# Kernel optimization log

Hardware: AMD Instinct MI355X
Metric: run time of the kernel (lower is better)

Reference implementation:

```python
import jax, jax.numpy as jnp
import numpy as np

D_KQ = 1024

def setup_inputs() -> dict:
    key = jax.random.key(0)
    k1, k2, k3, k4, k5 = jax.random.split(key, 5)
    x = jax.random.normal(k1, (4, 2048, 1024), dtype=jnp.float32)
    attention_mask = jax.random.randint(k2, (2048, 2048), 0, 2) == 1
    q_weights = jax.random.normal(k3, (1024, 1024), dtype=jnp.float32)
    k_weights = jax.random.normal(k4, (1024, 1024), dtype=jnp.float32)
    v_weights = jax.random.normal(k5, (1024, 1024), dtype=jnp.float32)
    return {"x": x, "attention_mask": attention_mask,
            "q_weights": q_weights, "k_weights": k_weights, "v_weights": v_weights}

def reference(x, attention_mask, q_weights, k_weights, v_weights):
    # projections: [B,S,d_in] @ [d_in,d] -> [B,S,d]
    query = x @ q_weights
    key = x @ k_weights
    value = x @ v_weights
    # scores: [B,S,S]
    attn_scores = jnp.einsum('bqd,bkd->bqk', query, key)
    masked = jnp.where(attention_mask, -jnp.inf, attn_scores)
    attn_weights = jax.nn.softmax(masked / jnp.sqrt(jnp.float32(D_KQ)), axis=-1)
    return attn_weights @ value
```

## Files before the change

kernel.cpp:

```cpp
#include <hip/hip_runtime.h>
#include <math.h>

static constexpr int BATCH = 4;
static constexpr int SEQ   = 2048;
static constexpr int DIM   = 1024;

typedef __attribute__((ext_vector_type(8))) short     bf16x8;
typedef __attribute__((ext_vector_type(4))) float     f32x4;

__device__ __forceinline__ unsigned short f2b(float v) {
    unsigned int u = __float_as_uint(v);
    u = u + 0x7fffu + ((u >> 16) & 1u);
    return (unsigned short)(u >> 16);
}
__device__ __forceinline__ float b2f(unsigned short h) {
    return __uint_as_float(((unsigned int)h) << 16);
}

__global__ __launch_bounds__(256) void convert_x_kernel(
    const float* __restrict__ X, unsigned short* __restrict__ hi,
    unsigned short* __restrict__ lo)
{
    const int i = blockIdx.x * 256 + threadIdx.x;
    const float4 v = ((const float4*)X)[i];
    ushort4 h, l;
    h.x = f2b(v.x); l.x = f2b(v.x - b2f(h.x));
    h.y = f2b(v.y); l.y = f2b(v.y - b2f(h.y));
    h.z = f2b(v.z); l.z = f2b(v.z - b2f(h.z));
    h.w = f2b(v.w); l.w = f2b(v.w - b2f(h.w));
    ((ushort4*)hi)[i] = h;
    ((ushort4*)lo)[i] = l;
}

__global__ __launch_bounds__(256) void convert_wqk_kernel(
    const float* __restrict__ Wq, const float* __restrict__ Wk,
    unsigned short* __restrict__ hi, unsigned short* __restrict__ lo)
{
    const int z = blockIdx.y;
    const float* __restrict__ W = z ? Wk : Wq;
    const int i = blockIdx.x * 256 + threadIdx.x;
    const int o = z * (DIM * DIM / 4) + i;
    const float4 v = ((const float4*)W)[i];
    ushort4 h, l;
    h.x = f2b(v.x); l.x = f2b(v.x - b2f(h.x));
    h.y = f2b(v.y); l.y = f2b(v.y - b2f(h.y));
    h.z = f2b(v.z); l.z = f2b(v.z - b2f(h.z));
    h.w = f2b(v.w); l.w = f2b(v.w - b2f(h.w));
    ((ushort4*)hi)[o] = h;
    ((ushort4*)lo)[o] = l;
}

__global__ __launch_bounds__(256) void convert_wv_kernel(
    const float* __restrict__ W, unsigned short* __restrict__ WT)
{
    __shared__ float t[32][33];
    const int n0 = blockIdx.x * 32, k0 = blockIdx.y * 32;
    const int tx = threadIdx.x & 31, ty = threadIdx.x >> 5;
#pragma unroll
    for (int i = 0; i < 4; ++i)
        t[ty + i * 8][tx] = W[(size_t)(k0 + ty + i * 8) * DIM + (n0 + tx)];
    __syncthreads();
#pragma unroll
    for (int i = 0; i < 4; ++i)
        WT[(size_t)(n0 + ty + i * 8) * DIM + (k0 + tx)] = f2b(t[tx][ty + i * 8]);
}

__global__ __launch_bounds__(256) void mask_pack_kernel(
    const int* __restrict__ mask, unsigned long long* __restrict__ Mb)
{
    const int row  = blockIdx.x;
    const int lane = threadIdx.x & 63, w = threadIdx.x >> 6;
#pragma unroll
    for (int c = w; c < SEQ / 64; c += 4) {
        const int v = mask[(size_t)row * SEQ + c * 64 + lane];
        const unsigned long long bits = __ballot(v != 0);
        if (lane == 0) Mb[(size_t)row * (SEQ / 64) + c] = bits;
    }
}

__device__ __forceinline__ void stage_async(
    const unsigned short* __restrict__ g, int gstride, int row0, int k0,
    unsigned short* lds, int tid)
{
    const int w = tid >> 6, lane = tid & 63;
    const int c = (lane & 3) ^ ((lane >> 4) & 3);
#pragma unroll
    for (int h = 0; h < 2; ++h) {
        const int row = 32 * w + 16 * h + (lane >> 2);
        const unsigned short* src = g + (size_t)(row0 + row) * gstride + k0 + 8 * c;
        unsigned short* dst = lds + (32 * w + 16 * h) * 32;
        __builtin_amdgcn_global_load_lds(
            (const __attribute__((address_space(1))) void*)src,
            (__attribute__((address_space(3))) void*)dst, 16, 0, 0);
    }
}

__device__ __forceinline__ bf16x8 fragr(const unsigned short* lds, int row, int qsw)
{
    return *(const bf16x8*)(lds + row * 32 + qsw * 8);
}

__global__ __launch_bounds__(256) void m_gemm_kernel(
    const unsigned short* __restrict__ Whi, const unsigned short* __restrict__ Wlo,
    float* __restrict__ Mtp)
{
    __shared__ unsigned short Ah[128 * 32], Al[128 * 32];
    __shared__ unsigned short Bh[128 * 32], Bl[128 * 32];

    const int tid = threadIdx.x;
    const int w = tid >> 6, lane = tid & 63;
    const int wm = (w >> 1) * 64, wn = (w & 1) * 64;
    const int m0 = blockIdx.y * 128, n0 = blockIdx.x * 128;
    const int z = blockIdx.z;

    const unsigned short* __restrict__ Ahg = Whi + (size_t)DIM * DIM;
    const unsigned short* __restrict__ Alg = Wlo + (size_t)DIM * DIM;
    const unsigned short* __restrict__ Bhg = Whi;
    const unsigned short* __restrict__ Blg = Wlo;
    float* __restrict__ Cp = Mtp + (size_t)z * DIM * DIM;

    f32x4 acc[4][4];
#pragma unroll
    for (int i = 0; i < 4; ++i)
#pragma unroll
        for (int j = 0; j < 4; ++j) acc[i][j] = (f32x4){0.f, 0.f, 0.f, 0.f};

    const int fr = lane & 15, quad = lane >> 4;
    const int qsw = quad ^ ((fr >> 2) & 3);

    for (int k0 = z * 256; k0 < z * 256 + 256; k0 += 32) {
        stage_async(Ahg, DIM, m0, k0, Ah, tid);
        stage_async(Alg, DIM, m0, k0, Al, tid);
        stage_async(Bhg, DIM, n0, k0, Bh, tid);
        stage_async(Blg, DIM, n0, k0, Bl, tid);
        __syncthreads();

        bf16x8 ah[4], al[4];
#pragma unroll
        for (int mt = 0; mt < 4; ++mt) {
            ah[mt] = fragr(Ah, wm + mt * 16 + fr, qsw);
            al[mt] = fragr(Al, wm + mt * 16 + fr, qsw);
        }
#pragma unroll
        for (int nt = 0; nt < 4; ++nt) {
            const bf16x8 bh = fragr(Bh, wn + nt * 16 + fr, qsw);
            const bf16x8 bl = fragr(Bl, wn + nt * 16 + fr, qsw);
#pragma unroll
            for (int mt = 0; mt < 4; ++mt) {
                acc[mt][nt] = __builtin_amdgcn_mfma_f32_16x16x32_bf16(ah[mt], bh, acc[mt][nt], 0, 0, 0);
                acc[mt][nt] = __builtin_amdgcn_mfma_f32_16x16x32_bf16(ah[mt], bl, acc[mt][nt], 0, 0, 0);
                acc[mt][nt] = __builtin_amdgcn_mfma_f32_16x16x32_bf16(al[mt], bh, acc[mt][nt], 0, 0, 0);
            }
        }
        __syncthreads();
    }

    const int col = lane & 15, rq = lane >> 4;
#pragma unroll
    for (int mt = 0; mt < 4; ++mt)
#pragma unroll
        for (int nt = 0; nt < 4; ++nt)
#pragma unroll
            for (int e = 0; e < 4; ++e) {
                const int m = m0 + wm + mt * 16 + rq * 4 + e;
                const int n = n0 + wn + nt * 16 + col;
                Cp[(size_t)m * DIM + n] = acc[mt][nt][e];
            }
}

__global__ __launch_bounds__(256) void m_reduce_kernel(
    const float* __restrict__ Mtp, unsigned short* __restrict__ Mthi,
    unsigned short* __restrict__ Mtlo)
{
    const int i = blockIdx.x * 256 + threadIdx.x;
    const size_t q = (size_t)DIM * DIM / 4;
    const float4 a = ((const float4*)Mtp)[i];
    const float4 b = ((const float4*)Mtp)[i + q];
    const float4 c = ((const float4*)Mtp)[i + 2 * q];
    const float4 d = ((const float4*)Mtp)[i + 3 * q];
    const float4 v = make_float4(a.x + b.x + c.x + d.x, a.y + b.y + c.y + d.y,
                                 a.z + b.z + c.z + d.z, a.w + b.w + c.w + d.w);
    ushort4 h, l;
    h.x = f2b(v.x); l.x = f2b(v.x - b2f(h.x));
    h.y = f2b(v.y); l.y = f2b(v.y - b2f(h.y));
    h.z = f2b(v.z); l.z = f2b(v.z - b2f(h.z));
    h.w = f2b(v.w); l.w = f2b(v.w - b2f(h.w));
    ((ushort4*)Mthi)[i] = h;
    ((ushort4*)Mtlo)[i] = l;
}

__global__ __launch_bounds__(256) void yv_gemm_kernel(
    const unsigned short* __restrict__ Xhi, const unsigned short* __restrict__ Xlo,
    const unsigned short* __restrict__ Mthi, const unsigned short* __restrict__ Mtlo,
    const unsigned short* __restrict__ WvT,
    unsigned short* __restrict__ Yhi, unsigned short* __restrict__ Ylo,
    unsigned short* __restrict__ Vt)
{
    __shared__ unsigned short Ah[128 * 32], Al[128 * 32];
    __shared__ unsigned short Bh[128 * 32], Bl[128 * 32];

    const int tid = threadIdx.x;
    const int w = tid >> 6, lane = tid & 63;
    const int wm = (w >> 1) * 64, wn = (w & 1) * 64;

    const int flat = blockIdx.x + (blockIdx.y << 3) + (blockIdx.z << 9);
    const int xcd = flat & 7, s = flat >> 3;
    const int cg  = xcd + ((s >> 3) << 3);
    const int n0 = (s & 7) * 128;
    const int m0 = (cg & 63) * 128;
    const int z  = cg >> 6;
    const bool full = (z == 0);

    const unsigned short* __restrict__ Bhg = full ? Mthi : WvT;
    const unsigned short* __restrict__ Blg = Mtlo;

    f32x4 acc[4][4];
#pragma unroll
    for (int i = 0; i < 4; ++i)
#pragma unroll
        for (int j = 0; j < 4; ++j) acc[i][j] = (f32x4){0.f, 0.f, 0.f, 0.f};

    const int fr = lane & 15, quad = lane >> 4;
    const int qsw = quad ^ ((fr >> 2) & 3);

    for (int k0 = 0; k0 < DIM; k0 += 32) {
        stage_async(Xhi, DIM, m0, k0, Ah, tid);
        stage_async(Bhg, DIM, n0, k0, Bh, tid);
        if (full) {
            stage_async(Xlo, DIM, m0, k0, Al, tid);
            stage_async(Blg, DIM, n0, k0, Bl, tid);
        }
        __syncthreads();

        bf16x8 ah[4], al[4];
#pragma unroll
        for (int mt = 0; mt < 4; ++mt)
            ah[mt] = fragr(Ah, wm + mt * 16 + fr, qsw);
        if (full) {
#pragma unroll
            for (int mt = 0; mt < 4; ++mt)
                al[mt] = fragr(Al, wm + mt * 16 + fr, qsw);
        }
#pragma unroll
        for (int nt = 0; nt < 4; ++nt) {
            const bf16x8 bh = fragr(Bh, wn + nt * 16 + fr, qsw);
#pragma unroll
            for (int mt = 0; mt < 4; ++mt)
                acc[mt][nt] = __builtin_amdgcn_mfma_f32_16x16x32_bf16(ah[mt], bh, acc[mt][nt], 0, 0, 0);
            if (full) {
                const bf16x8 bl = fragr(Bl, wn + nt * 16 + fr, qsw);
#pragma unroll
                for (int mt = 0; mt < 4; ++mt) {
                    acc[mt][nt] = __builtin_amdgcn_mfma_f32_16x16x32_bf16(ah[mt], bl, acc[mt][nt], 0, 0, 0);
                    acc[mt][nt] = __builtin_amdgcn_mfma_f32_16x16x32_bf16(al[mt], bh, acc[mt][nt], 0, 0, 0);
                }
            }
        }
        __syncthreads();
    }

    const int col = lane & 15, rq = lane >> 4;
    if (full) {
#pragma unroll
        for (int mt = 0; mt < 4; ++mt)
#pragma unroll
            for (int nt = 0; nt < 4; ++nt)
#pragma unroll
                for (int e = 0; e < 4; ++e) {
                    const int m = m0 + wm + mt * 16 + rq * 4 + e;
                    const int n = n0 + wn + nt * 16 + col;
                    const float v = acc[mt][nt][e];
                    const unsigned short h = f2b(v);
                    Yhi[(size_t)m * DIM + n] = h;
                    Ylo[(size_t)m * DIM + n] = f2b(v - b2f(h));
                }
    } else {
#pragma unroll
        for (int mt = 0; mt < 4; ++mt)
#pragma unroll
            for (int nt = 0; nt < 4; ++nt) {
                const int m = m0 + wm + mt * 16 + rq * 4;
                const int bb = m >> 11, sr = m & (SEQ - 1);
                const int n = n0 + wn + nt * 16 + col;
                ushort4 pk;
                pk.x = f2b(acc[mt][nt][0]);
                pk.y = f2b(acc[mt][nt][1]);
                pk.z = f2b(acc[mt][nt][2]);
                pk.w = f2b(acc[mt][nt][3]);
                *(ushort4*)(Vt + (size_t)bb * DIM * SEQ + (size_t)n * SEQ + sr) = pk;
            }
    }
}

__global__ __launch_bounds__(512, 2) void s_gemm256_kernel(
    const unsigned short* __restrict__ Yhi, const unsigned short* __restrict__ Ylo,
    const unsigned short* __restrict__ Xhi, const unsigned short* __restrict__ Xlo,
    const unsigned long long* __restrict__ Mb, float* __restrict__ Sc)
{
    extern __shared__ unsigned short smem[];

    const int tid = threadIdx.x;
    const int w = tid >> 6, lane = tid & 63;
    const int wm = (w >> 2) * 128, wn = (w & 3) * 64;

    const int flat = blockIdx.x + (blockIdx.y << 3) + (blockIdx.z << 6);
    const int lid  = ((flat & 7) << 5) | (flat >> 3);
    const int m0 = ((lid >> 3) & 7) * 256, n0 = (lid & 7) * 256;
    const int b  = lid >> 6;

    const unsigned short* __restrict__ Ahg = Yhi + (size_t)b * SEQ * DIM;
    const unsigned short* __restrict__ Alg = Ylo + (size_t)b * SEQ * DIM;
    const unsigned short* __restrict__ Bhg = Xhi + (size_t)b * SEQ * DIM;
    const unsigned short* __restrict__ Blg = Xlo + (size_t)b * SEQ * DIM;
    float* __restrict__ Sb = Sc + (size_t)b * SEQ * SEQ;

    f32x4 acc[8][4];
#pragma unroll
    for (int i = 0; i < 8; ++i)
#pragma unroll
        for (int j = 0; j < 4; ++j) acc[i][j] = (f32x4){0.f, 0.f, 0.f, 0.f};

    const int fr = lane & 15, quad = lane >> 4;
    const int qsw = quad ^ ((fr >> 2) & 3);

    stage_async(Ahg, DIM, m0, 0, smem + 0,     tid);
    stage_async(Bhg, DIM, n0, 0, smem + 16384, tid);
    stage_async(Blg, DIM, n0, 0, smem + 24576, tid);
    stage_async(Alg, DIM, m0, 0, smem + 8192,  tid);

    for (int it = 0; it < DIM / 32 - 1; ++it) {
        const int cur = (it & 1) * 32768;
        const int nxt = cur ^ 32768;
        const unsigned short* Ah = smem + cur;
        const unsigned short* Al = smem + cur + 8192;
        const unsigned short* Bh = smem + cur + 16384;
        const unsigned short* Bl = smem + cur + 24576;
        const int k1 = it * 32 + 32;

        bf16x8 ah[8], al[8], bh[4], bl[4];

        stage_async(Ahg, DIM, m0, k1, smem + nxt, tid);
        asm volatile("s_waitcnt vmcnt(6)" ::: "memory");
        __builtin_amdgcn_s_barrier();
#pragma unroll
        for (int mt = 0; mt < 4; ++mt)
            ah[mt] = fragr(Ah, wm + mt * 16 + fr, qsw);
#pragma unroll
        for (int nt = 0; nt < 4; ++nt)
            bh[nt] = fragr(Bh, wn + nt * 16 + fr, qsw);
        __builtin_amdgcn_s_setprio(1);
#pragma unroll
        for (int nt = 0; nt < 4; ++nt)
#pragma unroll
            for (int mt = 0; mt < 4; ++mt)
                acc[mt][nt] = __builtin_amdgcn_mfma_f32_16x16x32_bf16(ah[mt], bh[nt], acc[mt][nt], 0, 0, 0);
        __builtin_amdgcn_s_setprio(0);

        stage_async(Bhg, DIM, n0, k1, smem + nxt + 16384, tid);
#pragma unroll
        for (int mt = 4; mt < 8; ++mt)
            ah[mt] = fragr(Ah, wm + mt * 16 + fr, qsw);
        __builtin_amdgcn_s_setprio(1);
#pragma unroll
        for (int nt = 0; nt < 4; ++nt)
#pragma unroll
            for (int mt = 4; mt < 8; ++mt)
                acc[mt][nt] = __builtin_amdgcn_mfma_f32_16x16x32_bf16(ah[mt], bh[nt], acc[mt][nt], 0, 0, 0);
        __builtin_amdgcn_s_setprio(0);

        stage_async(Blg, DIM, n0, k1, smem + nxt + 24576, tid);
        asm volatile("s_waitcnt vmcnt(8)" ::: "memory");
        __builtin_amdgcn_s_barrier();
#pragma unroll
        for (int nt = 0; nt < 4; ++nt)
            bl[nt] = fragr(Bl, wn + nt * 16 + fr, qsw);
        __builtin_amdgcn_s_setprio(1);
#pragma unroll
        for (int nt = 0; nt < 4; ++nt)
#pragma unroll
            for (int mt = 0; mt < 4; ++mt)
                acc[mt][nt] = __builtin_amdgcn_mfma_f32_16x16x32_bf16(ah[mt], bl[nt], acc[mt][nt], 0, 0, 0);
        __builtin_amdgcn_s_setprio(0);

        __builtin_amdgcn_s_setprio(1);
#pragma unroll
        for (int nt = 0; nt < 4; ++nt)
#pragma unroll
            for (int mt = 4; mt < 8; ++mt)
                acc[mt][nt] = __builtin_amdgcn_mfma_f32_16x16x32_bf16(ah[mt], bl[nt], acc[mt][nt], 0, 0, 0);
        __builtin_amdgcn_s_setprio(0);

        stage_async(Alg, DIM, m0, k1, smem + nxt + 8192, tid);
        asm volatile("s_waitcnt vmcnt(8)" ::: "memory");
        __builtin_amdgcn_s_barrier();
#pragma unroll
        for (int mt = 0; mt < 4; ++mt)
            al[mt] = fragr(Al, wm + mt * 16 + fr, qsw);
        __builtin_amdgcn_s_setprio(1);
#pragma unroll
        for (int nt = 0; nt < 4; ++nt)
#pragma unroll
            for (int mt = 0; mt < 4; ++mt)
                acc[mt][nt] = __builtin_amdgcn_mfma_f32_16x16x32_bf16(al[mt], bh[nt], acc[mt][nt], 0, 0, 0);
        __builtin_amdgcn_s_setprio(0);

#pragma unroll
        for (int mt = 4; mt < 8; ++mt)
            al[mt] = fragr(Al, wm + mt * 16 + fr, qsw);
        __builtin_amdgcn_s_setprio(1);
#pragma unroll
        for (int nt = 0; nt < 4; ++nt)
#pragma unroll
            for (int mt = 4; mt < 8; ++mt)
                acc[mt][nt] = __builtin_amdgcn_mfma_f32_16x16x32_bf16(al[mt], bh[nt], acc[mt][nt], 0, 0, 0);
        __builtin_amdgcn_s_setprio(0);
    }

    {
        const unsigned short* Ah = smem + 32768;
        const unsigned short* Al = smem + 32768 + 8192;
        const unsigned short* Bh = smem + 32768 + 16384;
        const unsigned short* Bl = smem + 32768 + 24576;

        bf16x8 ah[8], al[8], bh[4], bl[4];

        asm volatile("s_waitcnt vmcnt(4)" ::: "memory");
        __builtin_amdgcn_s_barrier();
#pragma unroll
        for (int mt = 0; mt < 8; ++mt)
            ah[mt] = fragr(Ah, wm + mt * 16 + fr, qsw);
#pragma unroll
        for (int nt = 0; nt < 4; ++nt)
            bh[nt] = fragr(Bh, wn + nt * 16 + fr, qsw);
        __builtin_amdgcn_s_setprio(1);
#pragma unroll
        for (int nt = 0; nt < 4; ++nt)
#pragma unroll
            for (int mt = 0; mt < 8; ++mt)
                acc[mt][nt] = __builtin_amdgcn_mfma_f32_16x16x32_bf16(ah[mt], bh[nt], acc[mt][nt], 0, 0, 0);
        __builtin_amdgcn_s_setprio(0);

        asm volatile("s_waitcnt vmcnt(2)" ::: "memory");
        __builtin_amdgcn_s_barrier();
#pragma unroll
        for (int nt = 0; nt < 4; ++nt)
            bl[nt] = fragr(Bl, wn + nt * 16 + fr, qsw);
        __builtin_amdgcn_s_setprio(1);
#pragma unroll
        for (int nt = 0; nt < 4; ++nt)
#pragma unroll
            for (int mt = 0; mt < 8; ++mt)
                acc[mt][nt] = __builtin_amdgcn_mfma_f32_16x16x32_bf16(ah[mt], bl[nt], acc[mt][nt], 0, 0, 0);
        __builtin_amdgcn_s_setprio(0);

        asm volatile("s_waitcnt vmcnt(0)" ::: "memory");
        __builtin_amdgcn_s_barrier();
#pragma unroll
        for (int mt = 0; mt < 8; ++mt)
            al[mt] = fragr(Al, wm + mt * 16 + fr, qsw);
        __builtin_amdgcn_s_setprio(1);
#pragma unroll
        for (int nt = 0; nt < 4; ++nt)
#pragma unroll
            for (int mt = 0; mt < 8; ++mt)
                acc[mt][nt] = __builtin_amdgcn_mfma_f32_16x16x32_bf16(al[mt], bh[nt], acc[mt][nt], 0, 0, 0);
        __builtin_amdgcn_s_setprio(0);
    }

    const int col = lane & 15, rq = lane >> 4;
    const int wword = (n0 + wn) >> 6;
#pragma unroll
    for (int mt = 0; mt < 8; ++mt)
#pragma unroll
        for (int e = 0; e < 4; ++e) {
            const int m = m0 + wm + mt * 16 + rq * 4 + e;
            const unsigned long long word = Mb[(size_t)m * (SEQ / 64) + wword];
#pragma unroll
            for (int nt = 0; nt < 4; ++nt) {
                const int n = n0 + wn + nt * 16 + col;
                const float v = acc[mt][nt][e] * 0.03125f;
                const bool msk = (word >> (nt * 16 + col)) & 1ull;
                Sb[(size_t)m * SEQ + n] = msk ? -INFINITY : v;
            }
        }
}

__global__ __launch_bounds__(256) void softmax_kernel(float* __restrict__ Sc)
{
    const int r = blockIdx.x;
    float* __restrict__ row = Sc + (size_t)r * SEQ;

    const int tid  = threadIdx.x;
    const int lane = tid & 63;
    const int wid  = tid >> 6;

    float x[8];
    float mx = -INFINITY;
#pragma unroll
    for (int j = 0; j < 8; ++j) {
        x[j] = row[tid + j * 256];
        mx = fmaxf(mx, x[j]);
    }
    __shared__ float redm[4];
#pragma unroll
    for (int off = 32; off > 0; off >>= 1)
        mx = fmaxf(mx, __shfl_down(mx, off, 64));
    if (lane == 0) redm[wid] = mx;
    __syncthreads();
    mx = fmaxf(fmaxf(redm[0], redm[1]), fmaxf(redm[2], redm[3]));

    float sum = 0.f;
#pragma unroll
    for (int j = 0; j < 8; ++j) {
        const float e = __expf(x[j] - mx);
        x[j] = e;
        sum += e;
    }
    __shared__ float reds[4];
#pragma unroll
    for (int off = 32; off > 0; off >>= 1)
        sum += __shfl_down(sum, off, 64);
    if (lane == 0) reds[wid] = sum;
    __syncthreads();
    sum = (reds[0] + reds[1]) + (reds[2] + reds[3]);

    const float inv = 1.0f / sum;
    unsigned short* __restrict__ prow = (unsigned short*)row;
#pragma unroll
    for (int j = 0; j < 8; ++j)
        prow[tid + j * 256] = f2b(x[j] * inv);
}

__global__ __launch_bounds__(256) void pv_mfma_kernel(
    const unsigned short* __restrict__ P, const unsigned short* __restrict__ Vt,
    float* __restrict__ O)
{
    __shared__ unsigned short As[2][128 * 32], Bs[2][128 * 32];

    const int tid = threadIdx.x;
    const int w = tid >> 6, lane = tid & 63;
    const int wm = (w >> 1) * 64, wn = (w & 1) * 64;

    const int flat = blockIdx.x + (blockIdx.y << 3) + (blockIdx.z << 7);
    const int lid  = ((flat & 7) << 6) | (flat >> 3);
    const int m0 = ((lid >> 3) & 15) * 128, n0 = (lid & 7) * 128;
    const int b  = lid >> 7;

    const unsigned short* __restrict__ Ag = P + (size_t)b * SEQ * (2 * SEQ);
    const unsigned short* __restrict__ Bg = Vt + (size_t)b * DIM * SEQ;
    float* __restrict__ Ob = O + (size_t)b * SEQ * DIM;

    f32x4 acc[4][4];
#pragma unroll
    for (int i = 0; i < 4; ++i)
#pragma unroll
        for (int j = 0; j < 4; ++j) acc[i][j] = (f32x4){0.f, 0.f, 0.f, 0.f};

    const int fr = lane & 15, quad = lane >> 4;
    const int qsw = quad ^ ((fr >> 2) & 3);

    stage_async(Ag, 2 * SEQ, m0, 0, As[0], tid);
    stage_async(Bg, SEQ,     n0, 0, Bs[0], tid);

    for (int it = 0; it < SEQ / 32 - 1; ++it) {
        const int cur = it & 1, nxt = cur ^ 1;
        const int k1 = it * 32 + 32;

        stage_async(Ag, 2 * SEQ, m0, k1, As[nxt], tid);
        stage_async(Bg, SEQ,     n0, k1, Bs[nxt], tid);
        asm volatile("s_waitcnt vmcnt(4)" ::: "memory");
        __builtin_amdgcn_s_barrier();

        bf16x8 af[4];
#pragma unroll
        for (int mt = 0; mt < 4; ++mt)
            af[mt] = fragr(As[cur], wm + mt * 16 + fr, qsw);
        __builtin_amdgcn_s_setprio(1);
#pragma unroll
        for (int nt = 0; nt < 4; ++nt) {
            const bf16x8 bfg = fragr(Bs[cur], wn + nt * 16 + fr, qsw);
#pragma unroll
            for (int mt = 0; mt < 4; ++mt)
                acc[mt][nt] = __builtin_amdgcn_mfma_f32_16x16x32_bf16(af[mt], bfg, acc[mt][nt], 0, 0, 0);
        }
        __builtin_amdgcn_s_setprio(0);
        __builtin_amdgcn_s_barrier();
    }

    {
        asm volatile("s_waitcnt vmcnt(0)" ::: "memory");
        __builtin_amdgcn_s_barrier();
        bf16x8 af[4];
#pragma unroll
        for (int mt = 0; mt < 4; ++mt)
            af[mt] = fragr(As[1], wm + mt * 16 + fr, qsw);
        __builtin_amdgcn_s_setprio(1);
#pragma unroll
        for (int nt = 0; nt < 4; ++nt) {
            const bf16x8 bfg = fragr(Bs[1], wn + nt * 16 + fr, qsw);
#pragma unroll
            for (int mt = 0; mt < 4; ++mt)
                acc[mt][nt] = __builtin_amdgcn_mfma_f32_16x16x32_bf16(af[mt], bfg, acc[mt][nt], 0, 0, 0);
        }
        __builtin_amdgcn_s_setprio(0);
    }

    const int col = lane & 15, rq = lane >> 4;
#pragma unroll
    for (int mt = 0; mt < 4; ++mt)
#pragma unroll
        for (int nt = 0; nt < 4; ++nt)
#pragma unroll
            for (int e = 0; e < 4; ++e) {
                const int m = m0 + wm + mt * 16 + rq * 4 + e;
                const int n = n0 + wn + nt * 16 + col;
                Ob[(size_t)m * DIM + n] = acc[mt][nt][e];
            }
}

extern "C" void kernel_launch(void* const* d_in, const int* in_sizes, int n_in,
                              void* d_out, int out_size, void* d_ws, size_t ws_size,
                              hipStream_t stream)
{
    const float* x    = (const float*)d_in[0];
    const int*   mask = (const int*)d_in[1];
    const float* wq   = (const float*)d_in[2];
    const float* wk   = (const float*)d_in[3];
    const float* wv   = (const float*)d_in[4];
    float* out = (float*)d_out;

    const size_t NQ = (size_t)BATCH * SEQ * DIM;
    const size_t NM = (size_t)DIM * DIM;
    unsigned short* Xhi  = (unsigned short*)d_ws;
    unsigned short* Xlo  = Xhi + NQ;
    unsigned short* Yhi  = Xlo + NQ;
    unsigned short* Ylo  = Yhi + NQ;
    unsigned short* Vt   = Ylo + NQ;
    unsigned short* Mthi = Vt + NQ;
    unsigned short* Mtlo = Mthi + NM;
    float* Sc = (float*)(Mtlo + NM);
    unsigned long long* Mb = (unsigned long long*)(Sc + (size_t)BATCH * SEQ * SEQ);

    unsigned short* Whi = (unsigned short*)Sc;
    unsigned short* Wlo = Whi + 2 * NM;
    unsigned short* WvT = Wlo + 2 * NM;
    float* Mtp = (float*)(WvT + NM);

    static bool lds_attr_set = false;
    if (!lds_attr_set) {
        (void)hipFuncSetAttribute((const void*)s_gemm256_kernel,
                                  hipFuncAttributeMaxDynamicSharedMemorySize,
                                  131072);
        lds_attr_set = true;
    }

    convert_x_kernel<<<dim3(NQ / 4 / 256), 256, 0, stream>>>(x, Xhi, Xlo);
    mask_pack_kernel<<<dim3(SEQ), 256, 0, stream>>>(mask, Mb);
    convert_wqk_kernel<<<dim3(NM / 4 / 256, 2), 256, 0, stream>>>(wq, wk, Whi, Wlo);
    convert_wv_kernel<<<dim3(32, 32), 256, 0, stream>>>(wv, WvT);
    m_gemm_kernel<<<dim3(8, 8, 4), 256, 0, stream>>>(Whi, Wlo, Mtp);
    m_reduce_kernel<<<dim3(NM / 4 / 256), 256, 0, stream>>>(Mtp, Mthi, Mtlo);
    yv_gemm_kernel<<<dim3(DIM / 128, (BATCH * SEQ) / 128, 2), 256, 0, stream>>>(
        Xhi, Xlo, Mthi, Mtlo, WvT, Yhi, Ylo, Vt);
    s_gemm256_kernel<<<dim3(SEQ / 256, SEQ / 256, BATCH), 512, 131072, stream>>>(
        Yhi, Ylo, Xhi, Xlo, Mb, Sc);
    softmax_kernel<<<dim3(BATCH * SEQ), 256, 0, stream>>>(Sc);
    pv_mfma_kernel<<<dim3(DIM / 128, SEQ / 128, BATCH), 256, 0, stream>>>(
        (const unsigned short*)Sc, Vt, out);
}
```

Baseline: 371.2 us.

## Fuse Y and V projections into one double-buffered 256x128 GEMM kernel

The yv_gemm kernel used to compute the Y (split-bf16, three MFMA products) and V projections in separate blocks, each reloading the same X tile. It now computes both in one 512-thread block with 256x128 tiles, so X hi/lo are staged once and shared across the Y and V accumulators. Staging goes through double-buffered async global-to-LDS loads interleaved with MFMA phases, using explicit vmcnt waits, barriers and setprio. This adds register pressure from two accumulator sets and 112 KB of LDS per block, which limits occupancy, and the hand-tuned vmcnt counts make the pipeline fragile.

```diff
diff --git a/kernel.cpp b/kernel.cpp
--- a/kernel.cpp
+++ b/kernel.cpp
@@ -93,6 +93,20 @@
             (const __attribute__((address_space(1))) void*)src,
             (__attribute__((address_space(3))) void*)dst, 16, 0, 0);
     }
+}
+
+__device__ __forceinline__ void stage128(
+    const unsigned short* __restrict__ g, int gstride, int row0, int k0,
+    unsigned short* lds, int tid)
+{
+    const int w = tid >> 6, lane = tid & 63;
+    const int c = (lane & 3) ^ ((lane >> 4) & 3);
+    const int row = 16 * w + (lane >> 2);
+    const unsigned short* src = g + (size_t)(row0 + row) * gstride + k0 + 8 * c;
+    unsigned short* dst = lds + (16 * w) * 32;
+    __builtin_amdgcn_global_load_lds(
+        (const __attribute__((address_space(1))) void*)src,
+        (__attribute__((address_space(3))) void*)dst, 16, 0, 0);
 }
 
 __device__ __forceinline__ bf16x8 fragr(const unsigned short* lds, int row, int qsw)
@@ -189,107 +203,195 @@
     ((ushort4*)Mtlo)[i] = l;
 }
 
-__global__ __launch_bounds__(256) void yv_gemm_kernel(
+__global__ __launch_bounds__(512, 2) void yv_gemm_kernel(
     const unsigned short* __restrict__ Xhi, const unsigned short* __restrict__ Xlo,
     const unsigned short* __restrict__ Mthi, const unsigned short* __restrict__ Mtlo,
     const unsigned short* __restrict__ WvT,
     unsigned short* __restrict__ Yhi, unsigned short* __restrict__ Ylo,
     unsigned short* __restrict__ Vt)
 {
-    __shared__ unsigned short Ah[128 * 32], Al[128 * 32];
-    __shared__ unsigned short Bh[128 * 32], Bl[128 * 32];
+    extern __shared__ unsigned short smem[];
 
     const int tid = threadIdx.x;
     const int w = tid >> 6, lane = tid & 63;
     const int wm = (w >> 1) * 64, wn = (w & 1) * 64;
 
-    const int flat = blockIdx.x + (blockIdx.y << 3) + (blockIdx.z << 9);
+    const int flat = blockIdx.x + (blockIdx.y << 3);
     const int xcd = flat & 7, s = flat >> 3;
-    const int cg  = xcd + ((s >> 3) << 3);
+    const int m0 = (xcd + ((s >> 3) << 3)) * 256;
     const int n0 = (s & 7) * 128;
-    const int m0 = (cg & 63) * 128;
-    const int z  = cg >> 6;
-    const bool full = (z == 0);
-
-    const unsigned short* __restrict__ Bhg = full ? Mthi : WvT;
-    const unsigned short* __restrict__ Blg = Mtlo;
-
-    f32x4 acc[4][4];
+
+    f32x4 accY[4][4], accV[4][4];
 #pragma unroll
     for (int i = 0; i < 4; ++i)
 #pragma unroll
-        for (int j = 0; j < 4; ++j) acc[i][j] = (f32x4){0.f, 0.f, 0.f, 0.f};
+        for (int j = 0; j < 4; ++j) {
+            accY[i][j] = (f32x4){0.f, 0.f, 0.f, 0.f};
+            accV[i][j] = (f32x4){0.f, 0.f, 0.f, 0.f};
+        }
 
     const int fr = lane & 15, quad = lane >> 4;
     const int qsw = quad ^ ((fr >> 2) & 3);
 
-    for (int k0 = 0; k0 < DIM; k0 += 32) {
-        stage_async(Xhi, DIM, m0, k0, Ah, tid);
-        stage_async(Bhg, DIM, n0, k0, Bh, tid);
-        if (full) {
-            stage_async(Xlo, DIM, m0, k0, Al, tid);
-            stage_async(Blg, DIM, n0, k0, Bl, tid);
+    stage_async(Xhi, DIM, m0, 0, smem + 0,     tid);
+    stage128(Mthi, DIM, n0, 0, smem + 16384, tid);
+    stage128(Mtlo, DIM, n0, 0, smem + 20480, tid);
+    stage_async(Xlo, DIM, m0, 0, smem + 8192,  tid);
+    stage128(WvT,  DIM, n0, 0, smem + 24576, tid);
+
+    bf16x8 ah[4], al[4], bh[4], bl[4], bv[4];
+
+    for (int it = 0; it < DIM / 32 - 1; ++it) {
+        const int cur = (it & 1) * 28672;
+        const int nxt = 28672 - cur;
+        const int k1 = it * 32 + 32;
+
+        stage_async(Xhi, DIM, m0, k1, smem + nxt, tid);
+        asm volatile("s_waitcnt vmcnt(6)" ::: "memory");
+        __builtin_amdgcn_s_barrier();
+#pragma unroll
+        for (int mt = 0; mt < 4; ++mt)
+            ah[mt] = fragr(smem + cur, wm + mt * 16 + fr, qsw);
+#pragma unroll
+        for (int nt = 0; nt < 4; ++nt)
+            bh[nt] = fragr(smem + cur + 16384, wn + nt * 16 + fr, qsw);
+        __builtin_amdgcn_s_setprio(1);
+#pragma unroll
+        for (int nt = 0; nt < 4; ++nt)
+#pragma unroll
+            for (int mt = 0; mt < 4; ++mt)
+                accY[mt][nt] = __builtin_amdgcn_mfma_f32_16x16x32_bf16(ah[mt], bh[nt], accY[mt][nt], 0, 0, 0);
+        __builtin_amdgcn_s_setprio(0);
+
+        stage128(Mthi, DIM, n0, k1, smem + nxt + 16384, tid);
+        stage128(Mtlo, DIM, n0, k1, smem + nxt + 20480, tid);
+        asm volatile("s_waitcnt vmcnt(7)" ::: "memory");
+        __builtin_amdgcn_s_barrier();
+#pragma unroll
+        for (int nt = 0; nt < 4; ++nt)
+            bl[nt] = fragr(smem + cur + 20480, wn + nt * 16 + fr, qsw);
+        __builtin_amdgcn_s_setprio(1);
+#pragma unroll
+        for (int nt = 0; nt < 4; ++nt)
+#pragma unroll
+            for (int mt = 0; mt < 4; ++mt)
+                accY[mt][nt] = __builtin_amdgcn_mfma_f32_16x16x32_bf16(ah[mt], bl[nt], accY[mt][nt], 0, 0, 0);
+        __builtin_amdgcn_s_setprio(0);
+
+        stage_async(Xlo, DIM, m0, k1, smem + nxt + 8192, tid);
+        asm volatile("s_waitcnt vmcnt(6)" ::: "memory");
+        __builtin_amdgcn_s_barrier();
+#pragma unroll
+        for (int nt = 0; nt < 4; ++nt)
+            bv[nt] = fragr(smem + cur + 24576, wn + nt * 16 + fr, qsw);
+        __builtin_amdgcn_s_setprio(1);
+#pragma unroll
+        for (int nt = 0; nt < 4; ++nt)
+#pragma unroll
+            for (int mt = 0; mt < 4; ++mt)
+                accV[mt][nt] = __builtin_amdgcn_mfma_f32_16x16x32_bf16(ah[mt], bv[nt], accV[mt][nt], 0, 0, 0);
+        __builtin_amdgcn_s_setprio(0);
+
+        stage128(WvT, DIM, n0, k1, smem + nxt + 24576, tid);
+        asm volatile("s_waitcnt vmcnt(8)" ::: "memory");
+        __builtin_amdgcn_s_barrier();
+#pragma unroll
+        for (int mt = 0; mt < 4; ++mt)
+            al[mt] = fragr(smem + cur + 8192, wm + mt * 16 + fr, qsw);
+        __builtin_amdgcn_s_setprio(1);
+#pragma unroll
+        for (int nt = 0; nt < 4; ++nt)
+#pragma unroll
+            for (int mt = 0; mt < 4; ++mt)
+                accY[mt][nt] = __builtin_amdgcn_mfma_f32_16x16x32_bf16(al[mt], bh[nt], accY[mt][nt], 0, 0, 0);
+        __builtin_amdgcn_s_setprio(0);
+    }
+
+    {
+        const int cur = 28672;
+
+        asm volatile("s_waitcnt vmcnt(4)" ::: "memory");
+        __builtin_amdgcn_s_barrier();
+#pragma unroll
+        for (int mt = 0; mt < 4; ++mt)
+            ah[mt] = fragr(smem + cur, wm + mt * 16 + fr, qsw);
+#pragma unroll
+        for (int nt = 0; nt < 4; ++nt)
+            bh[nt] = fragr(smem + cur + 16384, wn + nt * 16 + fr, qsw);
+        __builtin_amdgcn_s_setprio(1);
+#pragma unroll
+        for (int nt = 0; nt < 4; ++nt)
+#pragma unroll
+            for (int mt = 0; mt < 4; ++mt)
+                accY[mt][nt] = __builtin_amdgcn_mfma_f32_16x16x32_bf16(ah[mt], bh[nt], accY[mt][nt], 0, 0, 0);
+        __builtin_amdgcn_s_setprio(0);
+
+        asm volatile("s_waitcnt vmcnt(3)" ::: "memory");
+        __builtin_amdgcn_s_barrier();
+#pragma unroll
+        for (int nt = 0; nt < 4; ++nt)
+            bl[nt] = fragr(smem + cur + 20480, wn + nt * 16 + fr, qsw);
+        __builtin_amdgcn_s_setprio(1);
+#pragma unroll
+        for (int nt = 0; nt < 4; ++nt)
+#pragma unroll
+            for (int mt = 0; mt < 4; ++mt)
+                accY[mt][nt] = __builtin_amdgcn_mfma_f32_16x16x32_bf16(ah[mt], bl[nt], accY[mt][nt], 0, 0, 0);
+        __builtin_amdgcn_s_setprio(0);
+
+        asm volatile("s_waitcnt vmcnt(0)" ::: "memory");
+        __builtin_amdgcn_s_barrier();
+#pragma unroll
+        for (int nt = 0; nt < 4; ++nt)
+            bv[nt] = fragr(smem + cur + 24576, wn + nt * 16 + fr, qsw);
+        __builtin_amdgcn_s_setprio(1);
+#pragma unroll
+        for (int nt = 0; nt < 4; ++nt)
+#pragma unroll
+            for (int mt = 0; mt < 4; ++mt)
+                accV[mt][nt] = __builtin_amdgcn_mfma_f32_16x16x32_bf16(ah[mt], bv[nt], accV[mt][nt], 0, 0, 0);
+        __builtin_amdgcn_s_setprio(0);
+
+#pragma unroll
+        for (int mt = 0; mt < 4; ++mt)
+            al[mt] = fragr(smem + cur + 8192, wm + mt * 16 + fr, qsw);
+        __builtin_amdgcn_s_setprio(1);
+#pragma unroll
+        for (int nt = 0; nt < 4; ++nt)
+#pragma unroll
+            for (int mt = 0; mt < 4; ++mt)
+                accY[mt][nt] = __builtin_amdgcn_mfma_f32_16x16x32_bf16(al[mt], bh[nt], accY[mt][nt], 0, 0, 0);
+        __builtin_amdgcn_s_setprio(0);
+    }
+
+    const int col = lane & 15, rq = lane >> 4;
+#pragma unroll
+    for (int mt = 0; mt < 4; ++mt)
+#pragma unroll
+        for (int nt = 0; nt < 4; ++nt)
+#pragma unroll
+            for (int e = 0; e < 4; ++e) {
+                const int m = m0 + wm + mt * 16 + rq * 4 + e;
+                const int n = n0 + wn + nt * 16 + col;
+                const float v = accY[mt][nt][e];
+                const unsigned short h = f2b(v);
+                Yhi[(size_t)m * DIM + n] = h;
+                Ylo[(size_t)m * DIM + n] = f2b(v - b2f(h));
+            }
+#pragma unroll
+    for (int mt = 0; mt < 4; ++mt)
+#pragma unroll
+        for (int nt = 0; nt < 4; ++nt) {
+            const int m = m0 + wm + mt * 16 + rq * 4;
+            const int bb = m >> 11, sr = m & (SEQ - 1);
+            const int n = n0 + wn + nt * 16 + col;
+            ushort4 pk;
+            pk.x = f2b(accV[mt][nt][0]);
+            pk.y = f2b(accV[mt][nt][1]);
+            pk.z = f2b(accV[mt][nt][2]);
+            pk.w = f2b(accV[mt][nt][3]);
+            *(ushort4*)(Vt + (size_t)bb * DIM * SEQ + (size_t)n * SEQ + sr) = pk;
         }
-        __syncthreads();
-
-        bf16x8 ah[4], al[4];
-#pragma unroll
-        for (int mt = 0; mt < 4; ++mt)
-            ah[mt] = fragr(Ah, wm + mt * 16 + fr, qsw);
-        if (full) {
-#pragma unroll
-            for (int mt = 0; mt < 4; ++mt)
-                al[mt] = fragr(Al, wm + mt * 16 + fr, qsw);
-        }
-#pragma unroll
-        for (int nt = 0; nt < 4; ++nt) {
-            const bf16x8 bh = fragr(Bh, wn + nt * 16 + fr, qsw);
-#pragma unroll
-            for (int mt = 0; mt < 4; ++mt)
-                acc[mt][nt] = __builtin_amdgcn_mfma_f32_16x16x32_bf16(ah[mt], bh, acc[mt][nt], 0, 0, 0);
-            if (full) {
-                const bf16x8 bl = fragr(Bl, wn + nt * 16 + fr, qsw);
-#pragma unroll
-                for (int mt = 0; mt < 4; ++mt) {
-                    acc[mt][nt] = __builtin_amdgcn_mfma_f32_16x16x32_bf16(ah[mt], bl, acc[mt][nt], 0, 0, 0);
-                    acc[mt][nt] = __builtin_amdgcn_mfma_f32_16x16x32_bf16(al[mt], bh, acc[mt][nt], 0, 0, 0);
-                }
-            }
-        }
-        __syncthreads();
-    }
-
-    const int col = lane & 15, rq = lane >> 4;
-    if (full) {
-#pragma unroll
-        for (int mt = 0; mt < 4; ++mt)
-#pragma unroll
-            for (int nt = 0; nt < 4; ++nt)
-#pragma unroll
-                for (int e = 0; e < 4; ++e) {
-                    const int m = m0 + wm + mt * 16 + rq * 4 + e;
-                    const int n = n0 + wn + nt * 16 + col;
-                    const float v = acc[mt][nt][e];
-                    const unsigned short h = f2b(v);
-                    Yhi[(size_t)m * DIM + n] = h;
-                    Ylo[(size_t)m * DIM + n] = f2b(v - b2f(h));
-                }
-    } else {
-#pragma unroll
-        for (int mt = 0; mt < 4; ++mt)
-#pragma unroll
-            for (int nt = 0; nt < 4; ++nt) {
-                const int m = m0 + wm + mt * 16 + rq * 4;
-                const int bb = m >> 11, sr = m & (SEQ - 1);
-                const int n = n0 + wn + nt * 16 + col;
-                ushort4 pk;
-                pk.x = f2b(acc[mt][nt][0]);
-                pk.y = f2b(acc[mt][nt][1]);
-                pk.z = f2b(acc[mt][nt][2]);
-                pk.w = f2b(acc[mt][nt][3]);
-                *(ushort4*)(Vt + (size_t)bb * DIM * SEQ + (size_t)n * SEQ + sr) = pk;
-            }
-    }
 }
 
 __global__ __launch_bounds__(512, 2) void s_gemm256_kernel(
@@ -651,6 +753,9 @@
         (void)hipFuncSetAttribute((const void*)s_gemm256_kernel,
                                   hipFuncAttributeMaxDynamicSharedMemorySize,
                                   131072);
+        (void)hipFuncSetAttribute((const void*)yv_gemm_kernel,
+                                  hipFuncAttributeMaxDynamicSharedMemorySize,
+                                  114688);
         lds_attr_set = true;
     }
 
@@ -660,7 +765,7 @@
     convert_wv_kernel<<<dim3(32, 32), 256, 0, stream>>>(wv, WvT);
     m_gemm_kernel<<<dim3(8, 8, 4), 256, 0, stream>>>(Whi, Wlo, Mtp);
     m_reduce_kernel<<<dim3(NM / 4 / 256), 256, 0, stream>>>(Mtp, Mthi, Mtlo);
-    yv_gemm_kernel<<<dim3(DIM / 128, (BATCH * SEQ) / 128, 2), 256, 0, stream>>>(
+    yv_gemm_kernel<<<dim3(DIM / 128, (BATCH * SEQ) / 256), 512, 114688, stream>>>(
         Xhi, Xlo, Mthi, Mtlo, WvT, Yhi, Ylo, Vt);
     s_gemm256_kernel<<<dim3(SEQ / 256, SEQ / 256, BATCH), 512, 131072, stream>>>(
         Yhi, Ylo, Xhi, Xlo, Mb, Sc);
```

Result: faster. 354.3 us (-4.6%).
